# Performance work log

Measured on AMD Instinct MI355X. Metric: run time of the kernel, lower is better.

The kernel has to match this reference:

```python
import jax, jax.numpy as jnp
import numpy as np

N = 8192      # number of tree nodes
K = 8         # max degree (8-ary tree)
ALPHA = 64    # alphabet size
DH = 256      # hidden dim


def _lin_w(key, din, dout):
    return jax.random.normal(key, (din, dout), jnp.float32) / np.sqrt(din)


def setup_inputs() -> dict:
    keys = jax.random.split(jax.random.key(0), 24)
    node_types = jax.random.randint(keys[0], (N,), 0, ALPHA, dtype=jnp.int32)
    # deterministic K-ary tree: children of node n are n*K+1 .. n*K+K (if < N)
    idx = np.arange(N)[:, None] * K + 1 + np.arange(K)[None, :]
    mask = idx < N
    children_np = np.where(mask, idx, 0).astype(np.int32)
    A_np = np.zeros((N, N), np.float32)
    A_np[np.repeat(np.arange(N), K)[mask.ravel()], idx.ravel()[mask.ravel()]] = 1.0
    return {
        "node_types": node_types,
        "children": jnp.asarray(children_np),
        "child_mask": jnp.asarray(mask),
        "A": jnp.asarray(A_np),
        # GCN layer params (self-transform + neighbor-transform)
        "Ws0": _lin_w(keys[1], ALPHA, DH), "Wn0": _lin_w(keys[2], ALPHA, DH), "b0": jnp.zeros((DH,), jnp.float32),
        "Ws1": _lin_w(keys[3], DH, DH),    "Wn1": _lin_w(keys[4], DH, DH),    "b1": jnp.zeros((DH,), jnp.float32),
        "Ws2": _lin_w(keys[5], DH, DH),    "Wn2": _lin_w(keys[6], DH, DH),    "b2": jnp.zeros((DH,), jnp.float32),
        # heads
        "we": _lin_w(keys[7], DH, 1), "be": jnp.zeros((1,), jnp.float32),
        "Wt": _lin_w(keys[8], DH, ALPHA), "bt": jnp.zeros((ALPHA,), jnp.float32),
        "ciu_w": _lin_w(keys[9], DH, 1)[:, 0], "ciu_b": jnp.zeros((), jnp.float32),
        "civ_w": _lin_w(keys[10], DH, 1)[:, 0], "civ_b": jnp.zeros((), jnp.float32),
        "ciw_w": jax.random.normal(keys[11], (), jnp.float32), "ciw_b": jnp.zeros((), jnp.float32),
        "cnu_w": _lin_w(keys[12], DH, 1)[:, 0], "cnu_b": jnp.zeros((), jnp.float32),
        "cnv_w": _lin_w(keys[13], DH, 1)[:, 0], "cnv_b": jnp.zeros((), jnp.float32),
        "cnw_w": jax.random.normal(keys[14], (), jnp.float32), "cnw_b": jnp.zeros((), jnp.float32),
    }


def reference(node_types, children, child_mask, A,
              Ws0, Wn0, b0, Ws1, Wn1, b1, Ws2, Wn2, b2,
              we, be, Wt, bt,
              ciu_w, ciu_b, civ_w, civ_b, ciw_w, ciw_b,
              cnu_w, cnu_b, cnv_w, cnv_b, cnw_w, cnw_b):
    X = jax.nn.one_hot(node_types, ALPHA, dtype=jnp.float32)  # [N, ALPHA]

    def gcn(Z, Ws, Wn, b):
        # self transform + adjacency-aggregated neighbor transform
        return Z @ Ws + b + A @ (Z @ Wn)

    H = jax.nn.relu(gcn(X, Ws0, Wn0, b0))
    H = jax.nn.relu(gcn(H, Ws1, Wn1, b1))
    H = jax.nn.relu(gcn(H, Ws2, Wn2, b2))  # [N, DH]

    delta = H @ we + be   # [N, 1] edit scores
    types = H @ Wt + bt   # [N, ALPHA]

    # child index / child num heads only for nodes with delta >= 0.5 and >0 children
    active = (delta[:, 0] >= 0.5) & child_mask.any(-1)
    valid = child_mask & active[:, None]          # [N, K]
    Hc = H[children]                               # [N, K, DH]
    dots = jnp.einsum('nkd,nd->nk', Hc, H)         # [N, K] child-parent products

    s_idx = (H @ ciu_w + ciu_b)[:, None] + (Hc @ civ_w + civ_b) + (ciw_w * dots + ciw_b)
    s_idx = jnp.where(valid, s_idx, 0.0)
    Cidx = jnp.zeros((N, K + 1), jnp.float32).at[:, 0].set(-1.0)
    # scores[i,1:deg+1] = s; scores[i,:deg] -= s  (s is zero-padded past deg)
    Cidx = Cidx.at[:, 1:].add(s_idx).at[:, :K].add(-s_idx)

    s_num = (H @ cnu_w + cnu_b)[:, None] + (Hc @ cnv_w + cnv_b) + (cnw_w * dots + cnw_b)
    Cnum = jnp.where(valid, s_num, 0.0)

    return delta, types, Cidx, Cnum
```

## Files before the change

### kernel.cpp

```cpp
#include <hip/hip_runtime.h>
#include <hip/hip_bf16.h>

#define N 8192
#define KDEG 8
#define ALPHA 64
#define DH 256

typedef unsigned short u16;
typedef __attribute__((ext_vector_type(8))) short short8;
typedef __attribute__((ext_vector_type(4))) float f32x4;
typedef __attribute__((ext_vector_type(4))) unsigned short ushort4_t;

__device__ __forceinline__ float wave_reduce_sum(float v) {
#pragma unroll
    for (int off = 32; off > 0; off >>= 1) v += __shfl_xor(v, off, 64);
    return v;
}
__device__ __forceinline__ u16 bf16_of(float x) {
    __hip_bfloat16 h = __float2bfloat16(x);
    return *(u16*)&h;
}
__device__ __forceinline__ float f_of_bf16(u16 u) {
    __hip_bfloat16 h = *(__hip_bfloat16*)&u;
    return __bfloat162float(h);
}


__global__ __launch_bounds__(256) void k_embed_pack(const int* __restrict__ nt,
    const float* __restrict__ Ws0, const float* __restrict__ Wn0, const float* __restrict__ b0,
    const float* __restrict__ Ws1, const float* __restrict__ Wn1,
    const float* __restrict__ Ws2, const float* __restrict__ Wn2,
    const float* __restrict__ Wt,
    u16* __restrict__ H0hi, u16* __restrict__ H0lo,
    u16* __restrict__ Phi, u16* __restrict__ Plo) {
    int tid = threadIdx.x;
    if (blockIdx.x < 2048) {
        int g = blockIdx.x * 256 + tid;
        int n = g >> 6, d = (g & 63) * 4;
        int t = nt[n];
        f32x4 a = *(const f32x4*)(b0 + d);
        a += *(const f32x4*)(Ws0 + t * DH + d);
        int cb = n * KDEG + 1;
#pragma unroll
        for (int i = 0; i < KDEG; i++) {
            int c = cb + i;
            if (c < N) a += *(const f32x4*)(Wn0 + nt[c] * DH + d);
        }
        ushort4_t hi, lo;
#pragma unroll
        for (int i = 0; i < 4; i++) {
            float x = fmaxf(a[i], 0.f);
            u16 h = bf16_of(x);
            hi[i] = h;
            lo[i] = bf16_of(x - f_of_bf16(h));
        }
        *(ushort4_t*)(H0hi + (size_t)n * DH + d) = hi;
        *(ushort4_t*)(H0lo + (size_t)n * DH + d) = lo;
    } else {
        int e = (blockIdx.x - 2048) * 256 + tid;
        if (e < 262144) {
            int m = e >> 17, o = e & 131071;
            int j = o & 7, l = (o >> 3) & 63, r = o >> 9;
            int kb = r & 15, tt = r >> 4;
            int k = kb * 32 + (l >> 4) * 8 + j;
            int c = tt * 16 + (l & 15);
            const float* W = (k < 256) ? (m ? Ws2 : Ws1) : (m ? Wn2 : Wn1);
            float v = W[(k & 255) * DH + c];
            u16 h = bf16_of(v);
            Phi[e] = h;
            Plo[e] = bf16_of(v - f_of_bf16(h));
        } else if (e < 278528) {
            int o = e - 262144;
            int j = o & 7, l = (o >> 3) & 63, r = o >> 9;
            int kb = r & 7, tt = r >> 3;
            int k = kb * 32 + (l >> 4) * 8 + j;
            int c = tt * 16 + (l & 15);
            float v = Wt[k * ALPHA + c];
            u16 h = bf16_of(v);
            Phi[e] = h;
            Plo[e] = bf16_of(v - f_of_bf16(h));
        }
    }
}

__global__ __launch_bounds__(256) void k_agg(const u16* __restrict__ Hhi,
                                             const u16* __restrict__ Hlo,
                                             u16* __restrict__ Aghi,
                                             u16* __restrict__ Aglo) {
    int n = blockIdx.x * 4 + (threadIdx.x >> 6);
    int d = (threadIdx.x & 63) * 4;
    f32x4 s = {};
    int cb = n * KDEG + 1;
#pragma unroll
    for (int i = 0; i < KDEG; i++) {
        int c = cb + i;
        if (c < N) {
            ushort4_t hi = *(const ushort4_t*)(Hhi + (size_t)c * DH + d);
            ushort4_t lo = *(const ushort4_t*)(Hlo + (size_t)c * DH + d);
#pragma unroll
            for (int q = 0; q < 4; q++) s[q] += f_of_bf16(hi[q]) + f_of_bf16(lo[q]);
        }
    }
    ushort4_t hi, lo;
#pragma unroll
    for (int q = 0; q < 4; q++) {
        u16 h = bf16_of(s[q]);
        hi[q] = h;
        lo[q] = bf16_of(s[q] - f_of_bf16(h));
    }
    *(ushort4_t*)(Aghi + (size_t)n * DH + d) = hi;
    *(ushort4_t*)(Aglo + (size_t)n * DH + d) = lo;
}

__global__ __launch_bounds__(256) void k_gemm(
    const u16* __restrict__ Hhi, const u16* __restrict__ Hlo,
    const u16* __restrict__ Aghi, const u16* __restrict__ Aglo,
    const u16* __restrict__ Pmhi, const u16* __restrict__ Pmlo,
    const float* __restrict__ bias,
    u16* __restrict__ Ohi, u16* __restrict__ Olo) {
    int w = blockIdx.x * 4 + (threadIdx.x >> 6);
    int lane = threadIdx.x & 63;
    int rg = w >> 3, cg = w & 7;
    int mrow = lane & 15, quad = lane >> 4;
    int row = rg * 16 + mrow;
    bool full = (rg < 64);

    const u16* hh = Hhi + (size_t)row * DH + quad * 8;
    const u16* hl = Hlo + (size_t)row * DH + quad * 8;

    f32x4 acc[2] = {};
#pragma unroll
    for (int kb = 0; kb < 8; kb++) {
        short8 ah = *(const short8*)(hh + kb * 32);
        short8 al = *(const short8*)(hl + kb * 32);
#pragma unroll
        for (int ct = 0; ct < 2; ct++) {
            size_t bo = ((size_t)((cg * 2 + ct) * 16 + kb) * 64 + lane) * 8;
            short8 bh = *(const short8*)(Pmhi + bo);
            short8 bl = *(const short8*)(Pmlo + bo);
            acc[ct] = __builtin_amdgcn_mfma_f32_16x16x32_bf16(ah, bh, acc[ct], 0, 0, 0);
            acc[ct] = __builtin_amdgcn_mfma_f32_16x16x32_bf16(ah, bl, acc[ct], 0, 0, 0);
            acc[ct] = __builtin_amdgcn_mfma_f32_16x16x32_bf16(al, bh, acc[ct], 0, 0, 0);
        }
    }
    if (full) {
        const u16* gh = Aghi + (size_t)row * DH + quad * 8;
        const u16* gl = Aglo + (size_t)row * DH + quad * 8;
#pragma unroll
        for (int kb = 0; kb < 8; kb++) {
            short8 ah = *(const short8*)(gh + kb * 32);
            short8 al = *(const short8*)(gl + kb * 32);
#pragma unroll
            for (int ct = 0; ct < 2; ct++) {
                size_t bo = ((size_t)((cg * 2 + ct) * 16 + kb + 8) * 64 + lane) * 8;
                short8 bh = *(const short8*)(Pmhi + bo);
                short8 bl = *(const short8*)(Pmlo + bo);
                acc[ct] = __builtin_amdgcn_mfma_f32_16x16x32_bf16(ah, bh, acc[ct], 0, 0, 0);
                acc[ct] = __builtin_amdgcn_mfma_f32_16x16x32_bf16(ah, bl, acc[ct], 0, 0, 0);
                acc[ct] = __builtin_amdgcn_mfma_f32_16x16x32_bf16(al, bh, acc[ct], 0, 0, 0);
            }
        }
    }
#pragma unroll
    for (int ct = 0; ct < 2; ct++) {
        int col = cg * 32 + ct * 16 + mrow;
        float bb = bias[col];
        int rowb = rg * 16 + quad * 4;
#pragma unroll
        for (int r = 0; r < 4; r++) {
            float x = fmaxf(acc[ct][r] + bb, 0.f);
            u16 h = bf16_of(x);
            Ohi[(size_t)(rowb + r) * DH + col] = h;
            Olo[(size_t)(rowb + r) * DH + col] = bf16_of(x - f_of_bf16(h));
        }
    }
}

__global__ __launch_bounds__(256) void k_scalars(const u16* __restrict__ Hhi,
                                                 const u16* __restrict__ Hlo,
                                                 const float* __restrict__ we,
                                                 const float* __restrict__ be,
                                                 const float* __restrict__ ciu_w,
                                                 const float* __restrict__ ciu_b,
                                                 const float* __restrict__ civ_w,
                                                 const float* __restrict__ civ_b,
                                                 const float* __restrict__ cnu_w,
                                                 const float* __restrict__ cnu_b,
                                                 const float* __restrict__ cnv_w,
                                                 const float* __restrict__ cnv_b,
                                                 float* __restrict__ aux,
                                                 float* __restrict__ delta_out) {
    int n = blockIdx.x * 4 + (threadIdx.x >> 6);
    int j = threadIdx.x & 63, d = j * 4;
    ushort4_t hi = *(const ushort4_t*)(Hhi + (size_t)n * DH + d);
    ushort4_t lo = *(const ushort4_t*)(Hlo + (size_t)n * DH + d);
    f32x4 x;
#pragma unroll
    for (int i = 0; i < 4; i++) x[i] = f_of_bf16(hi[i]) + f_of_bf16(lo[i]);
    f32x4 w0 = *(const f32x4*)(we + d);
    f32x4 w1 = *(const f32x4*)(ciu_w + d);
    f32x4 w2 = *(const f32x4*)(civ_w + d);
    f32x4 w3 = *(const f32x4*)(cnu_w + d);
    f32x4 w4 = *(const f32x4*)(cnv_w + d);
    float pd = 0.f, p1 = 0.f, p2 = 0.f, p3 = 0.f, p4 = 0.f;
#pragma unroll
    for (int i = 0; i < 4; i++) {
        pd += x[i] * w0[i];
        p1 += x[i] * w1[i];
        p2 += x[i] * w2[i];
        p3 += x[i] * w3[i];
        p4 += x[i] * w4[i];
    }
    pd = wave_reduce_sum(pd);
    p1 = wave_reduce_sum(p1);
    p2 = wave_reduce_sum(p2);
    p3 = wave_reduce_sum(p3);
    p4 = wave_reduce_sum(p4);
    if (j == 0) {
        float dv = pd + be[0];
        aux[n * 8 + 0] = dv;
        aux[n * 8 + 1] = p1 + ciu_b[0];
        aux[n * 8 + 2] = p2 + civ_b[0];
        aux[n * 8 + 3] = p3 + cnu_b[0];
        aux[n * 8 + 4] = p4 + cnv_b[0];
        delta_out[n] = dv;
    }
}

__global__ __launch_bounds__(256) void k_heads(const u16* __restrict__ Hhi,
                                               const u16* __restrict__ Hlo,
                                               const u16* __restrict__ Bh,
                                               const u16* __restrict__ Bl,
                                               const float* __restrict__ bt,
                                               const float* __restrict__ aux,
                                               const float* __restrict__ ciw_w,
                                               const float* __restrict__ ciw_b,
                                               const float* __restrict__ cnw_w,
                                               const float* __restrict__ cnw_b,
                                               float* __restrict__ types_out,
                                               float* __restrict__ cidx_out,
                                               float* __restrict__ cnum_out) {
    int lane = threadIdx.x & 63;
    if (blockIdx.x < 128) {
        int w = blockIdx.x * 4 + (threadIdx.x >> 6);
        int mrow = lane & 15, quad = lane >> 4;
        int r0 = w * 16;
        f32x4 acc[4] = {};
        const u16* ap = Hhi + (size_t)(r0 + mrow) * DH + quad * 8;
        const u16* lp = Hlo + (size_t)(r0 + mrow) * DH + quad * 8;
#pragma unroll
        for (int kb = 0; kb < 8; kb++) {
            short8 ah = *(const short8*)(ap + kb * 32);
            short8 al = *(const short8*)(lp + kb * 32);
#pragma unroll
            for (int ct = 0; ct < 4; ct++) {
                short8 bh = *(const short8*)(Bh + (size_t)((ct * 8 + kb) * 64 + lane) * 8);
                short8 bl = *(const short8*)(Bl + (size_t)((ct * 8 + kb) * 64 + lane) * 8);
                acc[ct] = __builtin_amdgcn_mfma_f32_16x16x32_bf16(ah, bh, acc[ct], 0, 0, 0);
                acc[ct] = __builtin_amdgcn_mfma_f32_16x16x32_bf16(ah, bl, acc[ct], 0, 0, 0);
                acc[ct] = __builtin_amdgcn_mfma_f32_16x16x32_bf16(al, bh, acc[ct], 0, 0, 0);
            }
        }
#pragma unroll
        for (int ct = 0; ct < 4; ct++) {
            float bias = bt[ct * 16 + mrow];
            int rowb = r0 + quad * 4;
#pragma unroll
            for (int r = 0; r < 4; r++)
                types_out[(size_t)(rowb + r) * ALPHA + ct * 16 + mrow] = acc[ct][r] + bias;
        }
    } else {
        int n = (blockIdx.x - 128) * 4 + (threadIdx.x >> 6);
        int j = lane, d = j * 4;
        ushort4_t phi = *(const ushort4_t*)(Hhi + (size_t)n * DH + d);
        ushort4_t plo = *(const ushort4_t*)(Hlo + (size_t)n * DH + d);
        float hp[4];
#pragma unroll
        for (int i = 0; i < 4; i++) hp[i] = f_of_bf16(phi[i]) + f_of_bf16(plo[i]);

        float delta = aux[n * 8 + 0];
        bool active = (delta >= 0.5f) && (n * KDEG + 1 < N);
        float ciu_n = aux[n * 8 + 1];
        float cnu_n = aux[n * 8 + 3];
        float iw = ciw_w[0], ib = ciw_b[0], nw = cnw_w[0], nb = cnw_b[0];

        float my_si = 0.f, my_sn = 0.f;
#pragma unroll
        for (int k = 0; k < KDEG; k++) {
            int c = n * KDEG + 1 + k;
            float si = 0.f, sn = 0.f;
            if (c < N) {
                ushort4_t chi = *(const ushort4_t*)(Hhi + (size_t)c * DH + d);
                ushort4_t clo = *(const ushort4_t*)(Hlo + (size_t)c * DH + d);
                float p = 0.f;
#pragma unroll
                for (int i = 0; i < 4; i++)
                    p += hp[i] * (f_of_bf16(chi[i]) + f_of_bf16(clo[i]));
                p = wave_reduce_sum(p);
                if (active) {
                    si = ciu_n + aux[c * 8 + 2] + iw * p + ib;
                    sn = cnu_n + aux[c * 8 + 4] + nw * p + nb;
                }
            }
            if (j == k) { my_si = si; my_sn = sn; }
        }
        if (j < KDEG) cnum_out[(size_t)n * KDEG + j] = my_sn;
        float prev = __shfl(my_si, (j >= 1) ? (j - 1) : 0, 64);
        float val;
        if (j == 0)        val = -1.f - my_si;
        else if (j < KDEG) val = prev - my_si;
        else               val = prev;
        if (j <= KDEG) cidx_out[(size_t)n * (KDEG + 1) + j] = val;
    }
}

extern "C" void kernel_launch(void* const* d_in, const int* in_sizes, int n_in,
                              void* d_out, int out_size, void* d_ws, size_t ws_size,
                              hipStream_t stream) {
    const int* nt = (const int*)d_in[0];
    const float* Ws0 = (const float*)d_in[4];
    const float* Wn0 = (const float*)d_in[5];
    const float* b0  = (const float*)d_in[6];
    const float* Ws1 = (const float*)d_in[7];
    const float* Wn1 = (const float*)d_in[8];
    const float* b1  = (const float*)d_in[9];
    const float* Ws2 = (const float*)d_in[10];
    const float* Wn2 = (const float*)d_in[11];
    const float* b2  = (const float*)d_in[12];
    const float* we  = (const float*)d_in[13];
    const float* be  = (const float*)d_in[14];
    const float* Wt  = (const float*)d_in[15];
    const float* bt  = (const float*)d_in[16];
    const float* ciu_w = (const float*)d_in[17];
    const float* ciu_b = (const float*)d_in[18];
    const float* civ_w = (const float*)d_in[19];
    const float* civ_b = (const float*)d_in[20];
    const float* ciw_w = (const float*)d_in[21];
    const float* ciw_b = (const float*)d_in[22];
    const float* cnu_w = (const float*)d_in[23];
    const float* cnu_b = (const float*)d_in[24];
    const float* cnv_w = (const float*)d_in[25];
    const float* cnv_b = (const float*)d_in[26];
    const float* cnw_w = (const float*)d_in[27];
    const float* cnw_b = (const float*)d_in[28];

    char* w = (char*)d_ws;
    u16* H0hi = (u16*)(w);
    u16* H0lo = (u16*)(w + ((size_t)4 << 20));
    u16* H1hi = (u16*)(w + ((size_t)8 << 20));
    u16* H1lo = (u16*)(w + ((size_t)12 << 20));
    u16* H2hi = (u16*)(w + ((size_t)16 << 20));
    u16* H2lo = (u16*)(w + ((size_t)20 << 20));
    u16* A0hi = (u16*)(w + ((size_t)24 << 20));
    u16* A0lo = (u16*)(w + ((size_t)25 << 20));
    u16* A1hi = (u16*)(w + ((size_t)26 << 20));
    u16* A1lo = (u16*)(w + ((size_t)27 << 20));
    float* aux = (float*)(w + ((size_t)28 << 20));
    u16* Phi = (u16*)(w + ((size_t)29 << 20));
    u16* Plo = (u16*)(w + ((size_t)30 << 20));

    float* delta_out = (float*)d_out;
    float* types_out = delta_out + N;
    float* cidx_out  = types_out + (size_t)N * ALPHA;
    float* cnum_out  = cidx_out + (size_t)N * (KDEG + 1);

    k_embed_pack<<<3136, 256, 0, stream>>>(nt, Ws0, Wn0, b0, Ws1, Wn1, Ws2, Wn2, Wt,
                                           H0hi, H0lo, Phi, Plo);
    k_agg<<<256, 256, 0, stream>>>(H0hi, H0lo, A0hi, A0lo);
    k_gemm<<<1024, 256, 0, stream>>>(H0hi, H0lo, A0hi, A0lo, Phi, Plo, b1, H1hi, H1lo);
    k_agg<<<256, 256, 0, stream>>>(H1hi, H1lo, A1hi, A1lo);
    k_gemm<<<1024, 256, 0, stream>>>(H1hi, H1lo, A1hi, A1lo,
                                     Phi + 131072, Plo + 131072, b2, H2hi, H2lo);
    k_scalars<<<2048, 256, 0, stream>>>(H2hi, H2lo, we, be, ciu_w, ciu_b, civ_w, civ_b,
                                        cnu_w, cnu_b, cnv_w, cnv_b, aux, delta_out);
    k_heads<<<128 + 2048, 256, 0, stream>>>(H2hi, H2lo, Phi + 262144, Plo + 262144, bt,
                                            aux, ciw_w, ciw_b, cnw_w, cnw_b,
                                            types_out, cidx_out, cnum_out);
}
```

Baseline: 407.5 us.

## Fuse child aggregation into GEMM blocks and fold scalar heads into k_heads

The separate aggregation kernel is merged into the GEMM kernel. Each 512-thread block first computes the child sums for its 16 rows, then synchronizes and runs the MFMA GEMM with 8 waves covering all output columns. The scalar-projection kernel and its aux buffer are removed. k_heads now computes delta and the ciu/civ/cnu/cnv projections inline, and does the child work only for active nodes. This cuts kernel launches and intermediate traffic, in exchange for extra wave reductions per child and a block-wide barrier inside the GEMM.

```diff
diff --git a/kernel.cpp b/kernel.cpp
--- a/kernel.cpp
+++ b/kernel.cpp
@@ -10,6 +10,7 @@
 typedef __attribute__((ext_vector_type(8))) short short8;
 typedef __attribute__((ext_vector_type(4))) float f32x4;
 typedef __attribute__((ext_vector_type(4))) unsigned short ushort4_t;
+typedef __attribute__((ext_vector_type(8))) unsigned short ushort8_t;
 
 __device__ __forceinline__ float wave_reduce_sum(float v) {
 #pragma unroll
@@ -83,47 +84,48 @@
     }
 }
 
-__global__ __launch_bounds__(256) void k_agg(const u16* __restrict__ Hhi,
-                                             const u16* __restrict__ Hlo,
-                                             u16* __restrict__ Aghi,
-                                             u16* __restrict__ Aglo) {
-    int n = blockIdx.x * 4 + (threadIdx.x >> 6);
-    int d = (threadIdx.x & 63) * 4;
-    f32x4 s = {};
-    int cb = n * KDEG + 1;
-#pragma unroll
-    for (int i = 0; i < KDEG; i++) {
-        int c = cb + i;
-        if (c < N) {
-            ushort4_t hi = *(const ushort4_t*)(Hhi + (size_t)c * DH + d);
-            ushort4_t lo = *(const ushort4_t*)(Hlo + (size_t)c * DH + d);
-#pragma unroll
-            for (int q = 0; q < 4; q++) s[q] += f_of_bf16(hi[q]) + f_of_bf16(lo[q]);
-        }
-    }
-    ushort4_t hi, lo;
-#pragma unroll
-    for (int q = 0; q < 4; q++) {
-        u16 h = bf16_of(s[q]);
-        hi[q] = h;
-        lo[q] = bf16_of(s[q] - f_of_bf16(h));
-    }
-    *(ushort4_t*)(Aghi + (size_t)n * DH + d) = hi;
-    *(ushort4_t*)(Aglo + (size_t)n * DH + d) = lo;
-}
-
-__global__ __launch_bounds__(256) void k_gemm(
+__global__ __launch_bounds__(512) void k_gemm_agg(
     const u16* __restrict__ Hhi, const u16* __restrict__ Hlo,
-    const u16* __restrict__ Aghi, const u16* __restrict__ Aglo,
+    u16* __restrict__ Ahi, u16* __restrict__ Alo,
     const u16* __restrict__ Pmhi, const u16* __restrict__ Pmlo,
     const float* __restrict__ bias,
     u16* __restrict__ Ohi, u16* __restrict__ Olo) {
-    int w = blockIdx.x * 4 + (threadIdx.x >> 6);
-    int lane = threadIdx.x & 63;
-    int rg = w >> 3, cg = w & 7;
+    int tid = threadIdx.x;
+    int rg = blockIdx.x;
+    if (rg < 64) {
+        int i = tid >> 5;
+        int cc = (tid & 31) * 8;
+        int node = rg * 16 + i;
+        int cb = node * KDEG + 1;
+        f32x4 s0 = {}, s1 = {};
+#pragma unroll
+        for (int k = 0; k < KDEG; k++) {
+            int c = cb + k;
+            if (c < N) {
+                ushort8_t hi = *(const ushort8_t*)(Hhi + (size_t)c * DH + cc);
+                ushort8_t lo = *(const ushort8_t*)(Hlo + (size_t)c * DH + cc);
+#pragma unroll
+                for (int q = 0; q < 4; q++) {
+                    s0[q] += f_of_bf16(hi[q]) + f_of_bf16(lo[q]);
+                    s1[q] += f_of_bf16(hi[4 + q]) + f_of_bf16(lo[4 + q]);
+                }
+            }
+        }
+        ushort8_t hi8, lo8;
+#pragma unroll
+        for (int q = 0; q < 4; q++) {
+            u16 h0 = bf16_of(s0[q]); hi8[q] = h0;     lo8[q] = bf16_of(s0[q] - f_of_bf16(h0));
+            u16 h1 = bf16_of(s1[q]); hi8[4 + q] = h1; lo8[4 + q] = bf16_of(s1[q] - f_of_bf16(h1));
+        }
+        *(ushort8_t*)(Ahi + (size_t)node * DH + cc) = hi8;
+        *(ushort8_t*)(Alo + (size_t)node * DH + cc) = lo8;
+    }
+    __syncthreads();
+
+    int cg = tid >> 6;
+    int lane = tid & 63;
     int mrow = lane & 15, quad = lane >> 4;
     int row = rg * 16 + mrow;
-    bool full = (rg < 64);
 
     const u16* hh = Hhi + (size_t)row * DH + quad * 8;
     const u16* hl = Hlo + (size_t)row * DH + quad * 8;
@@ -143,9 +145,9 @@
             acc[ct] = __builtin_amdgcn_mfma_f32_16x16x32_bf16(al, bh, acc[ct], 0, 0, 0);
         }
     }
-    if (full) {
-        const u16* gh = Aghi + (size_t)row * DH + quad * 8;
-        const u16* gl = Aglo + (size_t)row * DH + quad * 8;
+    if (rg < 64) {
+        const u16* gh = Ahi + (size_t)row * DH + quad * 8;
+        const u16* gl = Alo + (size_t)row * DH + quad * 8;
 #pragma unroll
         for (int kb = 0; kb < 8; kb++) {
             short8 ah = *(const short8*)(gh + kb * 32);
@@ -176,67 +178,26 @@
     }
 }
 
-__global__ __launch_bounds__(256) void k_scalars(const u16* __restrict__ Hhi,
-                                                 const u16* __restrict__ Hlo,
-                                                 const float* __restrict__ we,
-                                                 const float* __restrict__ be,
-                                                 const float* __restrict__ ciu_w,
-                                                 const float* __restrict__ ciu_b,
-                                                 const float* __restrict__ civ_w,
-                                                 const float* __restrict__ civ_b,
-                                                 const float* __restrict__ cnu_w,
-                                                 const float* __restrict__ cnu_b,
-                                                 const float* __restrict__ cnv_w,
-                                                 const float* __restrict__ cnv_b,
-                                                 float* __restrict__ aux,
-                                                 float* __restrict__ delta_out) {
-    int n = blockIdx.x * 4 + (threadIdx.x >> 6);
-    int j = threadIdx.x & 63, d = j * 4;
-    ushort4_t hi = *(const ushort4_t*)(Hhi + (size_t)n * DH + d);
-    ushort4_t lo = *(const ushort4_t*)(Hlo + (size_t)n * DH + d);
-    f32x4 x;
-#pragma unroll
-    for (int i = 0; i < 4; i++) x[i] = f_of_bf16(hi[i]) + f_of_bf16(lo[i]);
-    f32x4 w0 = *(const f32x4*)(we + d);
-    f32x4 w1 = *(const f32x4*)(ciu_w + d);
-    f32x4 w2 = *(const f32x4*)(civ_w + d);
-    f32x4 w3 = *(const f32x4*)(cnu_w + d);
-    f32x4 w4 = *(const f32x4*)(cnv_w + d);
-    float pd = 0.f, p1 = 0.f, p2 = 0.f, p3 = 0.f, p4 = 0.f;
-#pragma unroll
-    for (int i = 0; i < 4; i++) {
-        pd += x[i] * w0[i];
-        p1 += x[i] * w1[i];
-        p2 += x[i] * w2[i];
-        p3 += x[i] * w3[i];
-        p4 += x[i] * w4[i];
-    }
-    pd = wave_reduce_sum(pd);
-    p1 = wave_reduce_sum(p1);
-    p2 = wave_reduce_sum(p2);
-    p3 = wave_reduce_sum(p3);
-    p4 = wave_reduce_sum(p4);
-    if (j == 0) {
-        float dv = pd + be[0];
-        aux[n * 8 + 0] = dv;
-        aux[n * 8 + 1] = p1 + ciu_b[0];
-        aux[n * 8 + 2] = p2 + civ_b[0];
-        aux[n * 8 + 3] = p3 + cnu_b[0];
-        aux[n * 8 + 4] = p4 + cnv_b[0];
-        delta_out[n] = dv;
-    }
-}
-
 __global__ __launch_bounds__(256) void k_heads(const u16* __restrict__ Hhi,
                                                const u16* __restrict__ Hlo,
                                                const u16* __restrict__ Bh,
                                                const u16* __restrict__ Bl,
                                                const float* __restrict__ bt,
-                                               const float* __restrict__ aux,
+                                               const float* __restrict__ we,
+                                               const float* __restrict__ be,
+                                               const float* __restrict__ ciu_w,
+                                               const float* __restrict__ ciu_b,
+                                               const float* __restrict__ civ_w,
+                                               const float* __restrict__ civ_b,
+                                               const float* __restrict__ cnu_w,
+                                               const float* __restrict__ cnu_b,
+                                               const float* __restrict__ cnv_w,
+                                               const float* __restrict__ cnv_b,
                                                const float* __restrict__ ciw_w,
                                                const float* __restrict__ ciw_b,
                                                const float* __restrict__ cnw_w,
                                                const float* __restrict__ cnw_b,
+                                               float* __restrict__ delta_out,
                                                float* __restrict__ types_out,
                                                float* __restrict__ cidx_out,
                                                float* __restrict__ cnum_out) {
@@ -274,35 +235,51 @@
         int j = lane, d = j * 4;
         ushort4_t phi = *(const ushort4_t*)(Hhi + (size_t)n * DH + d);
         ushort4_t plo = *(const ushort4_t*)(Hlo + (size_t)n * DH + d);
-        float hp[4];
+        f32x4 hp;
 #pragma unroll
         for (int i = 0; i < 4; i++) hp[i] = f_of_bf16(phi[i]) + f_of_bf16(plo[i]);
 
-        float delta = aux[n * 8 + 0];
-        bool active = (delta >= 0.5f) && (n * KDEG + 1 < N);
-        float ciu_n = aux[n * 8 + 1];
-        float cnu_n = aux[n * 8 + 3];
-        float iw = ciw_w[0], ib = ciw_b[0], nw = cnw_w[0], nb = cnw_b[0];
-
+        f32x4 wd = *(const f32x4*)(we + d);
+        float pd = hp[0] * wd[0] + hp[1] * wd[1] + hp[2] * wd[2] + hp[3] * wd[3];
+        float delta = wave_reduce_sum(pd) + be[0];
+        if (j == 0) delta_out[n] = delta;
+
+        bool active = (delta >= 0.5f) && (n < 1024);
         float my_si = 0.f, my_sn = 0.f;
-#pragma unroll
-        for (int k = 0; k < KDEG; k++) {
-            int c = n * KDEG + 1 + k;
-            float si = 0.f, sn = 0.f;
-            if (c < N) {
-                ushort4_t chi = *(const ushort4_t*)(Hhi + (size_t)c * DH + d);
-                ushort4_t clo = *(const ushort4_t*)(Hlo + (size_t)c * DH + d);
-                float p = 0.f;
-#pragma unroll
-                for (int i = 0; i < 4; i++)
-                    p += hp[i] * (f_of_bf16(chi[i]) + f_of_bf16(clo[i]));
-                p = wave_reduce_sum(p);
-                if (active) {
-                    si = ciu_n + aux[c * 8 + 2] + iw * p + ib;
-                    sn = cnu_n + aux[c * 8 + 4] + nw * p + nb;
+        if (active) {
+            f32x4 w1 = *(const f32x4*)(ciu_w + d);
+            f32x4 w3 = *(const f32x4*)(cnu_w + d);
+            float ciu_n = wave_reduce_sum(hp[0] * w1[0] + hp[1] * w1[1] +
+                                          hp[2] * w1[2] + hp[3] * w1[3]) + ciu_b[0];
+            float cnu_n = wave_reduce_sum(hp[0] * w3[0] + hp[1] * w3[1] +
+                                          hp[2] * w3[2] + hp[3] * w3[3]) + cnu_b[0];
+            f32x4 w2 = *(const f32x4*)(civ_w + d);
+            f32x4 w4 = *(const f32x4*)(cnv_w + d);
+            float cvb = civ_b[0], nvb = cnv_b[0];
+            float iw = ciw_w[0], ib = ciw_b[0], nw = cnw_w[0], nb = cnw_b[0];
+#pragma unroll
+            for (int k = 0; k < KDEG; k++) {
+                int c = n * KDEG + 1 + k;
+                float si = 0.f, sn = 0.f;
+                if (c < N) {
+                    ushort4_t chi = *(const ushort4_t*)(Hhi + (size_t)c * DH + d);
+                    ushort4_t clo = *(const ushort4_t*)(Hlo + (size_t)c * DH + d);
+                    float p = 0.f, q2 = 0.f, q4 = 0.f;
+#pragma unroll
+                    for (int i = 0; i < 4; i++) {
+                        float hc = f_of_bf16(chi[i]) + f_of_bf16(clo[i]);
+                        p += hp[i] * hc;
+                        q2 += w2[i] * hc;
+                        q4 += w4[i] * hc;
+                    }
+                    p = wave_reduce_sum(p);
+                    q2 = wave_reduce_sum(q2);
+                    q4 = wave_reduce_sum(q4);
+                    si = ciu_n + (q2 + cvb) + iw * p + ib;
+                    sn = cnu_n + (q4 + nvb) + nw * p + nb;
                 }
+                if (j == k) { my_si = si; my_sn = sn; }
             }
-            if (j == k) { my_si = si; my_sn = sn; }
         }
         if (j < KDEG) cnum_out[(size_t)n * KDEG + j] = my_sn;
         float prev = __shfl(my_si, (j >= 1) ? (j - 1) : 0, 64);
@@ -355,9 +332,8 @@
     u16* A0lo = (u16*)(w + ((size_t)25 << 20));
     u16* A1hi = (u16*)(w + ((size_t)26 << 20));
     u16* A1lo = (u16*)(w + ((size_t)27 << 20));
-    float* aux = (float*)(w + ((size_t)28 << 20));
-    u16* Phi = (u16*)(w + ((size_t)29 << 20));
-    u16* Plo = (u16*)(w + ((size_t)30 << 20));
+    u16* Phi  = (u16*)(w + ((size_t)28 << 20));
+    u16* Plo  = (u16*)(w + ((size_t)29 << 20));
 
     float* delta_out = (float*)d_out;
     float* types_out = delta_out + N;
@@ -366,14 +342,12 @@
 
     k_embed_pack<<<3136, 256, 0, stream>>>(nt, Ws0, Wn0, b0, Ws1, Wn1, Ws2, Wn2, Wt,
                                            H0hi, H0lo, Phi, Plo);
-    k_agg<<<256, 256, 0, stream>>>(H0hi, H0lo, A0hi, A0lo);
-    k_gemm<<<1024, 256, 0, stream>>>(H0hi, H0lo, A0hi, A0lo, Phi, Plo, b1, H1hi, H1lo);
-    k_agg<<<256, 256, 0, stream>>>(H1hi, H1lo, A1hi, A1lo);
-    k_gemm<<<1024, 256, 0, stream>>>(H1hi, H1lo, A1hi, A1lo,
-                                     Phi + 131072, Plo + 131072, b2, H2hi, H2lo);
-    k_scalars<<<2048, 256, 0, stream>>>(H2hi, H2lo, we, be, ciu_w, ciu_b, civ_w, civ_b,
-                                        cnu_w, cnu_b, cnv_w, cnv_b, aux, delta_out);
+    k_gemm_agg<<<512, 512, 0, stream>>>(H0hi, H0lo, A0hi, A0lo, Phi, Plo, b1, H1hi, H1lo);
+    k_gemm_agg<<<512, 512, 0, stream>>>(H1hi, H1lo, A1hi, A1lo,
+                                        Phi + 131072, Plo + 131072, b2, H2hi, H2lo);
     k_heads<<<128 + 2048, 256, 0, stream>>>(H2hi, H2lo, Phi + 262144, Plo + 262144, bt,
-                                            aux, ciw_w, ciw_b, cnw_w, cnw_b,
-                                            types_out, cidx_out, cnum_out);
-}
+                                            we, be, ciu_w, ciu_b, civ_w, civ_b,
+                                            cnu_w, cnu_b, cnv_w, cnv_b,
+                                            ciw_w, ciw_b, cnw_w, cnw_b,
+                                            delta_out, types_out, cidx_out, cnum_out);
+}
```

Result: no change. 402.3 us (-1.3%).
